# Optimization experiments

Measured on AMD Instinct MI355X. Metric: run time of the kernel, lower is better.

Reference implementation:

```python
import jax, jax.numpy as jnp
import numpy as np

N, Lq, Lk = 4, 4096, 4096
H, P = 16, 128
D = H * P  # 2048


def setup_inputs() -> dict:
    key = jax.random.key(0)
    ks = jax.random.split(key, 7)
    s = 1.0 / np.sqrt(D).astype(np.float32)
    query = jax.random.normal(ks[0], (N, Lq, D), jnp.float32)
    key_t = jax.random.normal(ks[1], (N, Lk, D), jnp.float32)
    Wq = jax.random.normal(ks[2], (D, D), jnp.float32) * s
    Wk = jax.random.normal(ks[3], (D, D), jnp.float32) * s
    Wv = jax.random.normal(ks[4], (D, D), jnp.float32) * s
    query_padding_mask = jax.random.uniform(ks[5], (N, Lq)) < 0.1
    key_padding_mask = jax.random.uniform(ks[6], (N, Lk)) < 0.1
    return {"query": query, "key": key_t, "Wq": Wq, "Wk": Wk, "Wv": Wv,
            "query_padding_mask": query_padding_mask,
            "key_padding_mask": key_padding_mask}


def reference(query, key, Wq, Wk, Wv, query_padding_mask, key_padding_mask):
    n, lq, _ = query.shape
    lk = key.shape[1]
    # torch.nn.Linear(bias=False): y = x @ W^T; split into heads -> (N,H,L,P)
    q = (query @ Wq.T).reshape(n, lq, H, P).transpose(0, 2, 1, 3)
    k = (key @ Wk.T).reshape(n, lk, H, P).transpose(0, 2, 1, 3)
    v = (key @ Wv.T).reshape(n, lk, H, P).transpose(0, 2, 1, 3)
    # _log_exp_kernel(x) = log(1 + exp(x)) = softplus
    pq = jax.nn.softplus(q)
    pk = jax.nn.softplus(k)
    # zero out padded keys so they contribute nothing to numerator/denominator
    pk = jnp.where(key_padding_mask[:, None, :, None], 0.0, pk)
    # linear attention: O(L*d^2) instead of O(L^2*d)
    kv = jnp.einsum("nhkd,nhke->nhde", pk, v)          # (N,H,P,P)
    num = jnp.einsum("nhqd,nhde->nhqe", pq, kv)        # (N,H,Lq,P)
    den = jnp.einsum("nhqd,nhd->nhq", pq, pk.sum(axis=2))[..., None]
    att = num / den
    out = att.transpose(0, 2, 1, 3).reshape(n, lq, H * P)
    # zero out padded query positions
    out = jnp.where(query_padding_mask[..., None], 0.0, out)
    return out
```

## Files before the change

kernel.cpp:

```cpp
#include <hip/hip_runtime.h>
#include <stdint.h>

typedef __attribute__((ext_vector_type(8))) short    bh8;
typedef __attribute__((ext_vector_type(4))) float    fx4;
typedef __attribute__((ext_vector_type(4))) float    f4v;
typedef unsigned short u16;
typedef __attribute__((ext_vector_type(4))) unsigned short u16x4;

#define DEV static __device__ __forceinline__

DEV u16 f2bf(float f) {
  unsigned u = __float_as_uint(f);
  u += 0x7FFFu + ((u >> 16) & 1u);
  return (u16)(u >> 16);
}
DEV float bf2f(u16 s) { return __uint_as_float(((unsigned)s) << 16); }
DEV float softplus_f(float x) { return fmaxf(x, 0.f) + log1pf(expf(-fabsf(x))); }

DEV void gload_lds16(const u16* g, u16* l) {
  __builtin_amdgcn_global_load_lds(
      (const __attribute__((address_space(1))) unsigned int*)g,
      (__attribute__((address_space(3))) unsigned int*)l, 16, 0, 0);
}
DEV void stage2(const u16* s, u16* d) {
  gload_lds16(s, d);
  gload_lds16(s + 131072, d + 4096);
}

__global__ __launch_bounds__(256) void k_cvt(const float* __restrict__ in,
                                             u16* __restrict__ out, int n4) {
  int i = blockIdx.x * 256 + threadIdx.x;
  int stride = gridDim.x * 256;
  for (; i < n4; i += stride) {
    f4v v = ((const f4v*)in)[i];
    u16x4 o;
    o.x = f2bf(v.x); o.y = f2bf(v.y); o.z = f2bf(v.z); o.w = f2bf(v.w);
    ((u16x4*)out)[i] = o;
  }
}


#define MM(a, b, c) __builtin_amdgcn_mfma_f32_16x16x32_bf16(a, b, c, 0, 0, 0)
#define LD(BASE, RR, KS) \
  (*(const bh8*)&lsg[(BASE) + (RR) * 64 + ((((KS) * 32) + ko8) ^ swz)])

#define DECLQ(Q)                                                          \
  fx4 acc##Q##00 = {}, acc##Q##01 = {}, acc##Q##10 = {}, acc##Q##11 = {}, \
      acc##Q##20 = {}, acc##Q##21 = {}, acc##Q##30 = {}, acc##Q##31 = {}

#define DECLFRAGS                                                         \
  bh8 a_00 = {}, a_01 = {}, a_10 = {}, a_11 = {},                         \
      a_20 = {}, a_21 = {}, a_30 = {}, a_31 = {};                         \
  bh8 b0_00 = {}, b0_01 = {}, b0_10 = {}, b0_11 = {};                     \
  bh8 b1_00 = {}, b1_01 = {}, b1_10 = {}, b1_11 = {};

#define LDA4(AB, KS)                                                     \
  a_0##KS = LD(AB, arow0,      KS); a_1##KS = LD(AB, arow0 + 16, KS);    \
  a_2##KS = LD(AB, arow0 + 32, KS); a_3##KS = LD(AB, arow0 + 48, KS);

#define LDB2(BN, BB, KS)                                                 \
  b##BN##_0##KS = LD(BB, brow0,      KS);                                \
  b##BN##_1##KS = LD(BB, brow0 + 16, KS);

#define MFMA8(Q, BN, KS)                                                 \
  acc##Q##00 = MM(a_0##KS, b##BN##_0##KS, acc##Q##00);                   \
  acc##Q##01 = MM(a_0##KS, b##BN##_1##KS, acc##Q##01);                   \
  acc##Q##10 = MM(a_1##KS, b##BN##_0##KS, acc##Q##10);                   \
  acc##Q##11 = MM(a_1##KS, b##BN##_1##KS, acc##Q##11);                   \
  acc##Q##20 = MM(a_2##KS, b##BN##_0##KS, acc##Q##20);                   \
  acc##Q##21 = MM(a_2##KS, b##BN##_1##KS, acc##Q##21);                   \
  acc##Q##30 = MM(a_3##KS, b##BN##_0##KS, acc##Q##30);                   \
  acc##Q##31 = MM(a_3##KS, b##BN##_1##KS, acc##Q##31);

#define KREGION(ABASE, BBASE, DA, DB, SA, SB) {                          \
  stage2(SA,            lsu + (DA));                                     \
  stage2((SA) + 262144, lsu + (DA) + 8192);                              \
  stage2(SB,            lsu + (DB));                                     \
  stage2((SB) + 262144, lsu + (DB) + 8192);                              \
  LDA4(ABASE, 0) LDA4(ABASE, 1)                                          \
  LDB2(0, BBASE, 0) LDB2(0, BBASE, 1)                                    \
  LDB2(1, (BBASE) + 8192, 0) LDB2(1, (BBASE) + 8192, 1)                  \
  __builtin_amdgcn_s_setprio(1);                                         \
  MFMA8(0, 0, 0) MFMA8(0, 0, 1) MFMA8(1, 1, 0) MFMA8(1, 1, 1)            \
  LDA4((ABASE) + 8192, 0) LDA4((ABASE) + 8192, 1)                        \
  MFMA8(2, 0, 0) MFMA8(2, 0, 1) MFMA8(3, 1, 0) MFMA8(3, 1, 1)            \
  __builtin_amdgcn_s_setprio(0);                                         \
  asm volatile("s_waitcnt vmcnt(0)");                                    \
  __builtin_amdgcn_s_barrier();                                          \
}

#define STE(AC, EL, JOFF) {                                                   \
  float v = AC.EL;                                                            \
  if (EPI >= 1) v = softplus_f(v);                                            \
  if (EPI == 2) { if (mask[gi0 + JOFF]) v = 0.f; }                            \
  C[(size_t)(gi0 + JOFF) * 2048 + gj] = f2bf(v);                              \
}
#define ST1(AC, QR, QC, MI, NI) {                                             \
  int gi0 = bm0 + (QR) * 128 + wr * 64 + (MI) * 16 + (lane >> 4) * 4;         \
  int gj  = bn0 + (QC) * 128 + wc * 32 + (NI) * 16 + l15;                     \
  STE(AC, x, 0) STE(AC, y, 1) STE(AC, z, 2) STE(AC, w, 3)                     \
}
#define EPIQ(Q, QR, QC)                                                       \
  ST1(acc##Q##00, QR, QC, 0, 0) ST1(acc##Q##01, QR, QC, 0, 1)                 \
  ST1(acc##Q##10, QR, QC, 1, 0) ST1(acc##Q##11, QR, QC, 1, 1)                 \
  ST1(acc##Q##20, QR, QC, 2, 0) ST1(acc##Q##21, QR, QC, 2, 1)                 \
  ST1(acc##Q##30, QR, QC, 3, 0) ST1(acc##Q##31, QR, QC, 3, 1)

template <int EPI>
__global__ __launch_bounds__(512, 2) void k_gemm256(
    const u16* __restrict__ A, const u16* __restrict__ B, u16* __restrict__ C,
    const int* __restrict__ mask) {
  extern __shared__ u16 lsg[];
  int tid = threadIdx.x, lane = tid & 63, wid = tid >> 6;
  int xcd = blockIdx.x & 7, i = blockIdx.x >> 3;
  int bm0 = (xcd * 8 + (i & 7)) << 8;
  int bn0 = (i >> 3) << 8;
  int wr = wid >> 2, wc = wid & 3;
  int l15 = lane & 15, ko8 = (lane >> 4) * 8;
  int swz = (l15 & 7) << 3;
  int arow0 = wr * 64 + l15, brow0 = wc * 32 + l15;
  int lr = lane >> 3, cg = (lane & 7) ^ lr;
  const u16* srcA = A + (size_t)(bm0 + wid * 8 + lr) * 2048 + cg * 8;
  const u16* srcB = B + (size_t)(bn0 + wid * 8 + lr) * 2048 + cg * 8;
  u16* lsu = lsg + wid * 512;

  DECLQ(0); DECLQ(1); DECLQ(2); DECLQ(3);
  DECLFRAGS

  stage2(srcA,          lsu + 0);
  stage2(srcA + 262144, lsu + 8192);
  stage2(srcB,          lsu + 16384);
  stage2(srcB + 262144, lsu + 24576);
  asm volatile("s_waitcnt vmcnt(0)");
  __builtin_amdgcn_s_barrier();

  for (int it = 0; it < 16; it++) {
    const u16* sA1 = srcA + (2 * it + 1) * 64;
    const u16* sB1 = srcB + (2 * it + 1) * 64;
    int t2 = (2 * it + 2) & 31;
    const u16* sA2 = srcA + t2 * 64;
    const u16* sB2 = srcB + t2 * 64;
    KREGION(0,     16384, 32768, 49152, sA1, sB1)
    KREGION(32768, 49152, 0,     16384, sA2, sB2)
  }

  EPIQ(0, 0, 0)
  EPIQ(1, 0, 1)
  EPIQ(2, 1, 0)
  EPIQ(3, 1, 1)
}

__global__ __launch_bounds__(256, 2) void k_kv2(const u16* __restrict__ pk,
                                                const u16* __restrict__ v,
                                                float* __restrict__ part,
                                                float* __restrict__ spart) {
  int nh = blockIdx.x >> 3, slab = blockIdx.x & 7;
  int n = nh >> 4, h = nh & 15;
  __shared__ u16 lsA[128 * 32];
  __shared__ u16 lsB[128 * 32];
  __shared__ float redS[32][128];
  int tid = threadIdx.x, lane = tid & 63, wid = tid >> 6;
  int wr = wid >> 1, wc = wid & 1;
  int kk = tid >> 3;
  int dg = (tid & 7) * 16;
  size_t rowbase = ((size_t)(n * 4096 + slab * 512) + kk) * 2048 + h * 128 + dg;
  int r = lane & 15, ko = (lane >> 4) * 8;
  fx4 acc[4][4] = {};
  float sA[16];
#pragma unroll
  for (int i = 0; i < 16; i++) sA[i] = 0.f;
  for (int k0 = 0; k0 < 512; k0 += 32) {
    __syncthreads();
    bh8 a0 = *(const bh8*)(pk + rowbase + (size_t)k0 * 2048);
    bh8 a1 = *(const bh8*)(pk + rowbase + (size_t)k0 * 2048 + 8);
    bh8 b0 = *(const bh8*)(v + rowbase + (size_t)k0 * 2048);
    bh8 b1 = *(const bh8*)(v + rowbase + (size_t)k0 * 2048 + 8);
#pragma unroll
    for (int i = 0; i < 8; i++) {
      sA[i] += bf2f((u16)a0[i]);
      sA[8 + i] += bf2f((u16)a1[i]);
    }
#pragma unroll
    for (int i = 0; i < 8; i++) {
      lsA[(dg + i) * 32 + kk] = (u16)a0[i];
      lsA[(dg + 8 + i) * 32 + kk] = (u16)a1[i];
      lsB[(dg + i) * 32 + kk] = (u16)b0[i];
      lsB[(dg + 8 + i) * 32 + kk] = (u16)b1[i];
    }
    __syncthreads();
    bh8 af[4], bfr[4];
#pragma unroll
    for (int mi = 0; mi < 4; mi++)
      af[mi] = *(const bh8*)&lsA[(wr * 64 + mi * 16 + r) * 32 + ko];
#pragma unroll
    for (int ni = 0; ni < 4; ni++)
      bfr[ni] = *(const bh8*)&lsB[(wc * 64 + ni * 16 + r) * 32 + ko];
#pragma unroll
    for (int mi = 0; mi < 4; mi++)
#pragma unroll
      for (int ni = 0; ni < 4; ni++)
        acc[mi][ni] = __builtin_amdgcn_mfma_f32_16x16x32_bf16(af[mi], bfr[ni],
                                                              acc[mi][ni], 0, 0, 0);
  }
#pragma unroll
  for (int mi = 0; mi < 4; mi++)
#pragma unroll
    for (int ni = 0; ni < 4; ni++)
#pragma unroll
      for (int j = 0; j < 4; j++) {
        int d = wr * 64 + mi * 16 + (lane >> 4) * 4 + j;
        int e = wc * 64 + ni * 16 + (lane & 15);
        part[(size_t)blockIdx.x * 16384 + e * 128 + d] = acc[mi][ni][j];
      }
#pragma unroll
  for (int i = 0; i < 16; i++) redS[kk][dg + i] = sA[i];
  __syncthreads();
  if (tid < 128) {
    float s = 0.f;
#pragma unroll
    for (int p = 0; p < 32; p++) s += redS[p][tid];
    spart[blockIdx.x * 128 + tid] = s;
  }
}

__global__ __launch_bounds__(256) void k_red(const float* __restrict__ part,
                                             const float* __restrict__ spart,
                                             u16* __restrict__ kvT,
                                             float* __restrict__ sb) {
  int nh = blockIdx.x, tid = threadIdx.x;
  for (int i = tid; i < 16384; i += 256) {
    float s = 0.f;
#pragma unroll
    for (int sl = 0; sl < 8; sl++) s += part[(size_t)(nh * 8 + sl) * 16384 + i];
    kvT[(size_t)nh * 16384 + i] = f2bf(s);
  }
  if (tid < 128) {
    float s = 0.f;
#pragma unroll
    for (int sl = 0; sl < 8; sl++) s += spart[(nh * 8 + sl) * 128 + tid];
    sb[nh * 128 + tid] = s;
  }
}

__global__ __launch_bounds__(256, 2) void k_att(
    const u16* __restrict__ pq, const u16* __restrict__ kvT,
    const float* __restrict__ s, const int* __restrict__ qmask,
    float* __restrict__ out) {
  int b = blockIdx.x;
  int lt = b & 31, h = (b >> 5) & 15, nb = b >> 9;
  int l0 = lt * 128;
  __shared__ u16 lsQ[128 * 128];
  __shared__ u16 lsKV[128 * 128];
  __shared__ float lsS[128];
  __shared__ float lsDen[128];
  int tid = threadIdx.x, lane = tid & 63, wid = tid >> 6;

  int row = tid >> 1, part = tid & 1;
  const u16* gq = pq + ((size_t)(nb * 4096 + l0 + row)) * 2048 + h * 128 + part * 64;
  const u16* gk = kvT + ((size_t)(nb * 16 + h) * 128 + row) * 128 + part * 64;
  int sw = (row & 7) << 3;
#pragma unroll
  for (int j = 0; j < 8; j++) {
    bh8 vq = *(const bh8*)(gq + j * 8);
    bh8 vk = *(const bh8*)(gk + j * 8);
    int ci = (part * 64 + j * 8) ^ sw;
    *(bh8*)&lsQ[row * 128 + ci] = vq;
    *(bh8*)&lsKV[row * 128 + ci] = vk;
  }
  if (tid < 128) lsS[tid] = s[(nb * 16 + h) * 128 + tid];
  __syncthreads();

  if (tid < 128) {
    int rr = tid, swr = (rr & 7) << 3;
    float dsum = 0.f;
    for (int dd = 0; dd < 128; dd++) {
      int d = (dd + rr) & 127;
      dsum += bf2f(lsQ[rr * 128 + (d ^ swr)]) * lsS[d];
    }
    lsDen[rr] = dsum;
  }
  __syncthreads();

  int wr = wid >> 1, wc = wid & 1;
  int r = lane & 15, ko = (lane >> 4) * 8;
  fx4 acc[4][4] = {};
#pragma unroll
  for (int ks = 0; ks < 4; ks++) {
    bh8 af[4], bfr[4];
#pragma unroll
    for (int mi = 0; mi < 4; mi++) {
      int rw = wr * 64 + mi * 16 + r;
      af[mi] = *(const bh8*)&lsQ[rw * 128 + ((ks * 32 + ko) ^ ((rw & 7) << 3))];
    }
#pragma unroll
    for (int ni = 0; ni < 4; ni++) {
      int rw = wc * 64 + ni * 16 + r;
      bfr[ni] = *(const bh8*)&lsKV[rw * 128 + ((ks * 32 + ko) ^ ((rw & 7) << 3))];
    }
#pragma unroll
    for (int mi = 0; mi < 4; mi++)
#pragma unroll
      for (int ni = 0; ni < 4; ni++)
        acc[mi][ni] = __builtin_amdgcn_mfma_f32_16x16x32_bf16(af[mi], bfr[ni],
                                                              acc[mi][ni], 0, 0, 0);
  }
#pragma unroll
  for (int mi = 0; mi < 4; mi++)
#pragma unroll
    for (int ni = 0; ni < 4; ni++)
#pragma unroll
      for (int j = 0; j < 4; j++) {
        int li = wr * 64 + mi * 16 + (lane >> 4) * 4 + j;
        int e = wc * 64 + ni * 16 + (lane & 15);
        int l = l0 + li;
        float v = qmask[nb * 4096 + l] ? 0.f : acc[mi][ni][j] / lsDen[li];
        out[((size_t)(nb * 4096 + l)) * 2048 + h * 128 + e] = v;
      }
}

extern "C" void kernel_launch(void* const* d_in, const int* in_sizes, int n_in,
                              void* d_out, int out_size, void* d_ws, size_t ws_size,
                              hipStream_t stream) {
  const float* query = (const float*)d_in[0];
  const float* key   = (const float*)d_in[1];
  const float* Wq    = (const float*)d_in[2];
  const float* Wk    = (const float*)d_in[3];
  const float* Wv    = (const float*)d_in[4];
  const int* qmask   = (const int*)d_in[5];
  const int* kmask   = (const int*)d_in[6];
  float* out = (float*)d_out;
  char* ws = (char*)d_ws;

  u16* qb   = (u16*)(ws + 0);
  u16* kb   = (u16*)(ws + 67108864ull);
  u16* Wqb  = (u16*)(ws + 134217728ull);
  u16* Wkb  = (u16*)(ws + 142606336ull);
  u16* Wvb  = (u16*)(ws + 150994944ull);
  u16* pq   = (u16*)(ws + 159383552ull);
  u16* kvT  = (u16*)(ws + 226492416ull);
  float* sb = (float*)(ws + 228589568ull);
  float* kvpart = (float*)(ws + 0);
  float* spart  = (float*)(ws + 33554432ull);
  u16* pk = (u16*)d_out;
  u16* vb = (u16*)d_out + 33554432ull;

  k_cvt<<<2048, 256, 0, stream>>>(query, qb, 33554432 / 4);
  k_cvt<<<2048, 256, 0, stream>>>(key, kb, 33554432 / 4);
  k_cvt<<<512, 256, 0, stream>>>(Wq, Wqb, 4194304 / 4);
  k_cvt<<<512, 256, 0, stream>>>(Wk, Wkb, 4194304 / 4);
  k_cvt<<<512, 256, 0, stream>>>(Wv, Wvb, 4194304 / 4);

  k_gemm256<1><<<512, 512, 131072, stream>>>(qb, Wqb, pq, nullptr);
  k_gemm256<2><<<512, 512, 131072, stream>>>(kb, Wkb, pk, kmask);
  k_gemm256<0><<<512, 512, 131072, stream>>>(kb, Wvb, vb, nullptr);

  k_kv2<<<512, 256, 0, stream>>>(pk, vb, kvpart, spart);
  k_red<<<64, 256, 0, stream>>>(kvpart, spart, kvT, sb);
  k_att<<<2048, 256, 0, stream>>>(pq, kvT, sb, qmask, out);
}
```

Measured before the change: 740.9 us.

## Shrink projection GEMM tiles to 128x128 and merge fp32-to-bf16 conversions

The three projection GEMMs move from 256x256 tiles with 512 threads and 128KB LDS to 128x128 tiles with 256 threads and 64KB LDS, launched as 2048 blocks. Staging and the per-wave B fragment layout change to match. The five separate fp32-to-bf16 conversion launches become one kernel that relies on the workspace buffers being contiguous. Smaller tiles give more blocks and more resident blocks per CU, but each block reuses its loaded data less, so global and L2 traffic per FLOP roughly doubles.

Measured after the change: 819.5 us. 10.6% more time.

```diff
diff --git a/kernel.cpp b/kernel.cpp
--- a/kernel.cpp
+++ b/kernel.cpp
@@ -22,20 +22,31 @@
       (const __attribute__((address_space(1))) unsigned int*)g,
       (__attribute__((address_space(3))) unsigned int*)l, 16, 0, 0);
 }
-DEV void stage2(const u16* s, u16* d) {
+DEV void stage4(const u16* s, u16* d) {
   gload_lds16(s, d);
+  gload_lds16(s + 65536,  d + 2048);
   gload_lds16(s + 131072, d + 4096);
-}
-
-__global__ __launch_bounds__(256) void k_cvt(const float* __restrict__ in,
-                                             u16* __restrict__ out, int n4) {
+  gload_lds16(s + 196608, d + 6144);
+}
+
+__global__ __launch_bounds__(256) void k_cvt_all(
+    const float* __restrict__ q, const float* __restrict__ k,
+    const float* __restrict__ wq, const float* __restrict__ wk,
+    const float* __restrict__ wv, u16* __restrict__ dst) {
+  const int N4 = 19922944;
   int i = blockIdx.x * 256 + threadIdx.x;
   int stride = gridDim.x * 256;
-  for (; i < n4; i += stride) {
-    f4v v = ((const f4v*)in)[i];
+  for (; i < N4; i += stride) {
+    const float* src; int off;
+    if (i < 8388608)        { src = q;  off = i; }
+    else if (i < 16777216)  { src = k;  off = i - 8388608; }
+    else if (i < 17825792)  { src = wq; off = i - 16777216; }
+    else if (i < 18874368)  { src = wk; off = i - 17825792; }
+    else                    { src = wv; off = i - 18874368; }
+    f4v v = ((const f4v*)src)[off];
     u16x4 o;
     o.x = f2bf(v.x); o.y = f2bf(v.y); o.z = f2bf(v.z); o.w = f2bf(v.w);
-    ((u16x4*)out)[i] = o;
+    ((u16x4*)dst)[i] = o;
   }
 }
 
@@ -58,9 +69,9 @@
   a_0##KS = LD(AB, arow0,      KS); a_1##KS = LD(AB, arow0 + 16, KS);    \
   a_2##KS = LD(AB, arow0 + 32, KS); a_3##KS = LD(AB, arow0 + 48, KS);
 
-#define LDB2(BN, BB, KS)                                                 \
-  b##BN##_0##KS = LD(BB, brow0,      KS);                                \
-  b##BN##_1##KS = LD(BB, brow0 + 16, KS);
+#define LDB4(BN, BB, KS)                                                 \
+  b##BN##_0##KS = LD(BB, brow0 + (BN) * 32,      KS);                    \
+  b##BN##_1##KS = LD(BB, brow0 + (BN) * 32 + 16, KS);
 
 #define MFMA8(Q, BN, KS)                                                 \
   acc##Q##00 = MM(a_0##KS, b##BN##_0##KS, acc##Q##00);                   \
@@ -72,21 +83,18 @@
   acc##Q##30 = MM(a_3##KS, b##BN##_0##KS, acc##Q##30);                   \
   acc##Q##31 = MM(a_3##KS, b##BN##_1##KS, acc##Q##31);
 
-#define KREGION(ABASE, BBASE, DA, DB, SA, SB) {                          \
-  stage2(SA,            lsu + (DA));                                     \
-  stage2((SA) + 262144, lsu + (DA) + 8192);                              \
-  stage2(SB,            lsu + (DB));                                     \
-  stage2((SB) + 262144, lsu + (DB) + 8192);                              \
-  LDA4(ABASE, 0) LDA4(ABASE, 1)                                          \
-  LDB2(0, BBASE, 0) LDB2(0, BBASE, 1)                                    \
-  LDB2(1, (BBASE) + 8192, 0) LDB2(1, (BBASE) + 8192, 1)                  \
-  __builtin_amdgcn_s_setprio(1);                                         \
-  MFMA8(0, 0, 0) MFMA8(0, 0, 1) MFMA8(1, 1, 0) MFMA8(1, 1, 1)            \
-  LDA4((ABASE) + 8192, 0) LDA4((ABASE) + 8192, 1)                        \
-  MFMA8(2, 0, 0) MFMA8(2, 0, 1) MFMA8(3, 1, 0) MFMA8(3, 1, 1)            \
-  __builtin_amdgcn_s_setprio(0);                                         \
-  asm volatile("s_waitcnt vmcnt(0)");                                    \
-  __builtin_amdgcn_s_barrier();                                          \
+#define KTILE(AB, BB, SA, SB, DA, DB) {      \
+  stage4(SA, lsu + (DA));                    \
+  stage4(SB, lsu + (DB));                    \
+  LDA4(AB, 0) LDA4(AB, 1)                    \
+  LDB4(0, BB, 0) LDB4(0, BB, 1)              \
+  LDB4(1, BB, 0) LDB4(1, BB, 1)              \
+  __builtin_amdgcn_s_setprio(1);             \
+  MFMA8(0, 0, 0) MFMA8(0, 0, 1)              \
+  MFMA8(1, 1, 0) MFMA8(1, 1, 1)              \
+  __builtin_amdgcn_s_setprio(0);             \
+  asm volatile("s_waitcnt vmcnt(0)");        \
+  __builtin_amdgcn_s_barrier();              \
 }
 
 #define STE(AC, EL, JOFF) {                                                   \
@@ -95,42 +103,40 @@
   if (EPI == 2) { if (mask[gi0 + JOFF]) v = 0.f; }                            \
   C[(size_t)(gi0 + JOFF) * 2048 + gj] = f2bf(v);                              \
 }
-#define ST1(AC, QR, QC, MI, NI) {                                             \
-  int gi0 = bm0 + (QR) * 128 + wr * 64 + (MI) * 16 + (lane >> 4) * 4;         \
-  int gj  = bn0 + (QC) * 128 + wc * 32 + (NI) * 16 + l15;                     \
+#define ST1(AC, MI, NJ) {                                                     \
+  int gi0 = bm0 + wr * 64 + (MI) * 16 + (lane >> 4) * 4;                      \
+  int gj  = bn0 + wc * 64 + (NJ) * 16 + l15;                                  \
   STE(AC, x, 0) STE(AC, y, 1) STE(AC, z, 2) STE(AC, w, 3)                     \
 }
-#define EPIQ(Q, QR, QC)                                                       \
-  ST1(acc##Q##00, QR, QC, 0, 0) ST1(acc##Q##01, QR, QC, 0, 1)                 \
-  ST1(acc##Q##10, QR, QC, 1, 0) ST1(acc##Q##11, QR, QC, 1, 1)                 \
-  ST1(acc##Q##20, QR, QC, 2, 0) ST1(acc##Q##21, QR, QC, 2, 1)                 \
-  ST1(acc##Q##30, QR, QC, 3, 0) ST1(acc##Q##31, QR, QC, 3, 1)
+#define EPIQ(Q, NB)                                                           \
+  ST1(acc##Q##00, 0, NB) ST1(acc##Q##01, 0, (NB) + 1)                         \
+  ST1(acc##Q##10, 1, NB) ST1(acc##Q##11, 1, (NB) + 1)                         \
+  ST1(acc##Q##20, 2, NB) ST1(acc##Q##21, 2, (NB) + 1)                         \
+  ST1(acc##Q##30, 3, NB) ST1(acc##Q##31, 3, (NB) + 1)
 
 template <int EPI>
-__global__ __launch_bounds__(512, 2) void k_gemm256(
+__global__ __launch_bounds__(256, 2) void k_gemm128(
     const u16* __restrict__ A, const u16* __restrict__ B, u16* __restrict__ C,
     const int* __restrict__ mask) {
   extern __shared__ u16 lsg[];
   int tid = threadIdx.x, lane = tid & 63, wid = tid >> 6;
   int xcd = blockIdx.x & 7, i = blockIdx.x >> 3;
-  int bm0 = (xcd * 8 + (i & 7)) << 8;
-  int bn0 = (i >> 3) << 8;
-  int wr = wid >> 2, wc = wid & 3;
+  int bm0 = (xcd * 16 + (i >> 4)) << 7;
+  int bn0 = (i & 15) << 7;
+  int wr = wid >> 1, wc = wid & 1;
   int l15 = lane & 15, ko8 = (lane >> 4) * 8;
   int swz = (l15 & 7) << 3;
-  int arow0 = wr * 64 + l15, brow0 = wc * 32 + l15;
+  int arow0 = wr * 64 + l15, brow0 = wc * 64 + l15;
   int lr = lane >> 3, cg = (lane & 7) ^ lr;
   const u16* srcA = A + (size_t)(bm0 + wid * 8 + lr) * 2048 + cg * 8;
   const u16* srcB = B + (size_t)(bn0 + wid * 8 + lr) * 2048 + cg * 8;
   u16* lsu = lsg + wid * 512;
 
-  DECLQ(0); DECLQ(1); DECLQ(2); DECLQ(3);
+  DECLQ(0); DECLQ(1);
   DECLFRAGS
 
-  stage2(srcA,          lsu + 0);
-  stage2(srcA + 262144, lsu + 8192);
-  stage2(srcB,          lsu + 16384);
-  stage2(srcB + 262144, lsu + 24576);
+  stage4(srcA, lsu + 0);
+  stage4(srcB, lsu + 8192);
   asm volatile("s_waitcnt vmcnt(0)");
   __builtin_amdgcn_s_barrier();
 
@@ -140,14 +146,12 @@
     int t2 = (2 * it + 2) & 31;
     const u16* sA2 = srcA + t2 * 64;
     const u16* sB2 = srcB + t2 * 64;
-    KREGION(0,     16384, 32768, 49152, sA1, sB1)
-    KREGION(32768, 49152, 0,     16384, sA2, sB2)
-  }
-
-  EPIQ(0, 0, 0)
-  EPIQ(1, 0, 1)
-  EPIQ(2, 1, 0)
-  EPIQ(3, 1, 1)
+    KTILE(0,     8192,  sA1, sB1, 16384, 24576)
+    KTILE(16384, 24576, sA2, sB2, 0,     8192)
+  }
+
+  EPIQ(0, 0)
+  EPIQ(1, 2)
 }
 
 __global__ __launch_bounds__(256, 2) void k_kv2(const u16* __restrict__ pk,
@@ -344,15 +348,11 @@
   u16* pk = (u16*)d_out;
   u16* vb = (u16*)d_out + 33554432ull;
 
-  k_cvt<<<2048, 256, 0, stream>>>(query, qb, 33554432 / 4);
-  k_cvt<<<2048, 256, 0, stream>>>(key, kb, 33554432 / 4);
-  k_cvt<<<512, 256, 0, stream>>>(Wq, Wqb, 4194304 / 4);
-  k_cvt<<<512, 256, 0, stream>>>(Wk, Wkb, 4194304 / 4);
-  k_cvt<<<512, 256, 0, stream>>>(Wv, Wvb, 4194304 / 4);
-
-  k_gemm256<1><<<512, 512, 131072, stream>>>(qb, Wqb, pq, nullptr);
-  k_gemm256<2><<<512, 512, 131072, stream>>>(kb, Wkb, pk, kmask);
-  k_gemm256<0><<<512, 512, 131072, stream>>>(kb, Wvb, vb, nullptr);
+  k_cvt_all<<<2048, 256, 0, stream>>>(query, key, Wq, Wk, Wv, qb);
+
+  k_gemm128<1><<<2048, 256, 65536, stream>>>(qb, Wqb, pq, nullptr);
+  k_gemm128<2><<<2048, 256, 65536, stream>>>(kb, Wkb, pk, kmask);
+  k_gemm128<0><<<2048, 256, 65536, stream>>>(kb, Wvb, vb, nullptr);
 
   k_kv2<<<512, 256, 0, stream>>>(pk, vb, kvpart, spart);
   k_red<<<64, 256, 0, stream>>>(kvpart, spart, kvT, sb);
```

## Restructure GEMM main loop into double-buffered register/LDS pipeline and fuse conversions

Applied to the files above, without the earlier changes.

The GEMM main loop is reorganised so that LDS fragment reads for the next k-slice go into a second register set while MFMAs consume the current set, with global-to-LDS staging issued one slice ahead across two LDS buffers. The aim is to hide LDS read latency and global load latency behind matrix-core work instead of waiting inside each region. The five separate fp32-to-bf16 conversion launches are merged into one kernel over a contiguous destination, which removes launch overhead. The cost is a doubled fragment register footprint, which may pressure occupancy at two blocks per CU, plus more delicate waitcnt and barrier ordering.

Result: slower. 807.0 us (+8.9%).

```diff
diff --git a/kernel.cpp b/kernel.cpp
--- a/kernel.cpp
+++ b/kernel.cpp
@@ -27,15 +27,24 @@
   gload_lds16(s + 131072, d + 4096);
 }
 
-__global__ __launch_bounds__(256) void k_cvt(const float* __restrict__ in,
-                                             u16* __restrict__ out, int n4) {
+__global__ __launch_bounds__(256) void k_cvt_all(
+    const float* __restrict__ q, const float* __restrict__ k,
+    const float* __restrict__ wq, const float* __restrict__ wk,
+    const float* __restrict__ wv, u16* __restrict__ dst) {
+  const int N4 = 19922944;
   int i = blockIdx.x * 256 + threadIdx.x;
   int stride = gridDim.x * 256;
-  for (; i < n4; i += stride) {
-    f4v v = ((const f4v*)in)[i];
+  for (; i < N4; i += stride) {
+    const float* src; int off;
+    if (i < 8388608)        { src = q;  off = i; }
+    else if (i < 16777216)  { src = k;  off = i - 8388608; }
+    else if (i < 17825792)  { src = wq; off = i - 16777216; }
+    else if (i < 18874368)  { src = wk; off = i - 17825792; }
+    else                    { src = wv; off = i - 18874368; }
+    f4v v = ((const f4v*)src)[off];
     u16x4 o;
     o.x = f2bf(v.x); o.y = f2bf(v.y); o.z = f2bf(v.z); o.w = f2bf(v.w);
-    ((u16x4*)out)[i] = o;
+    ((u16x4*)dst)[i] = o;
   }
 }
 
@@ -48,45 +57,58 @@
   fx4 acc##Q##00 = {}, acc##Q##01 = {}, acc##Q##10 = {}, acc##Q##11 = {}, \
       acc##Q##20 = {}, acc##Q##21 = {}, acc##Q##30 = {}, acc##Q##31 = {}
 
-#define DECLFRAGS                                                         \
-  bh8 a_00 = {}, a_01 = {}, a_10 = {}, a_11 = {},                         \
-      a_20 = {}, a_21 = {}, a_30 = {}, a_31 = {};                         \
-  bh8 b0_00 = {}, b0_01 = {}, b0_10 = {}, b0_11 = {};                     \
-  bh8 b1_00 = {}, b1_01 = {}, b1_10 = {}, b1_11 = {};
-
-#define LDA4(AB, KS)                                                     \
-  a_0##KS = LD(AB, arow0,      KS); a_1##KS = LD(AB, arow0 + 16, KS);    \
-  a_2##KS = LD(AB, arow0 + 32, KS); a_3##KS = LD(AB, arow0 + 48, KS);
-
-#define LDB2(BN, BB, KS)                                                 \
-  b##BN##_0##KS = LD(BB, brow0,      KS);                                \
-  b##BN##_1##KS = LD(BB, brow0 + 16, KS);
-
-#define MFMA8(Q, BN, KS)                                                 \
-  acc##Q##00 = MM(a_0##KS, b##BN##_0##KS, acc##Q##00);                   \
-  acc##Q##01 = MM(a_0##KS, b##BN##_1##KS, acc##Q##01);                   \
-  acc##Q##10 = MM(a_1##KS, b##BN##_0##KS, acc##Q##10);                   \
-  acc##Q##11 = MM(a_1##KS, b##BN##_1##KS, acc##Q##11);                   \
-  acc##Q##20 = MM(a_2##KS, b##BN##_0##KS, acc##Q##20);                   \
-  acc##Q##21 = MM(a_2##KS, b##BN##_1##KS, acc##Q##21);                   \
-  acc##Q##30 = MM(a_3##KS, b##BN##_0##KS, acc##Q##30);                   \
-  acc##Q##31 = MM(a_3##KS, b##BN##_1##KS, acc##Q##31);
-
-#define KREGION(ABASE, BBASE, DA, DB, SA, SB) {                          \
-  stage2(SA,            lsu + (DA));                                     \
-  stage2((SA) + 262144, lsu + (DA) + 8192);                              \
-  stage2(SB,            lsu + (DB));                                     \
-  stage2((SB) + 262144, lsu + (DB) + 8192);                              \
-  LDA4(ABASE, 0) LDA4(ABASE, 1)                                          \
-  LDB2(0, BBASE, 0) LDB2(0, BBASE, 1)                                    \
-  LDB2(1, (BBASE) + 8192, 0) LDB2(1, (BBASE) + 8192, 1)                  \
-  __builtin_amdgcn_s_setprio(1);                                         \
-  MFMA8(0, 0, 0) MFMA8(0, 0, 1) MFMA8(1, 1, 0) MFMA8(1, 1, 1)            \
-  LDA4((ABASE) + 8192, 0) LDA4((ABASE) + 8192, 1)                        \
-  MFMA8(2, 0, 0) MFMA8(2, 0, 1) MFMA8(3, 1, 0) MFMA8(3, 1, 1)            \
-  __builtin_amdgcn_s_setprio(0);                                         \
-  asm volatile("s_waitcnt vmcnt(0)");                                    \
-  __builtin_amdgcn_s_barrier();                                          \
+#define DECLSET(S)                                                        \
+  bh8 aA##S##0 = {}, aA##S##1 = {}, aA##S##2 = {}, aA##S##3 = {},         \
+      aB##S##0 = {}, aB##S##1 = {}, aB##S##2 = {}, aB##S##3 = {},         \
+      b0##S##0 = {}, b0##S##1 = {}, b1##S##0 = {}, b1##S##1 = {};
+
+#define RD(S, BUF, KS)                                                       \
+  aA##S##0 = LD((BUF),         arow0,      KS);                              \
+  aA##S##1 = LD((BUF),         arow0 + 16, KS);                              \
+  aA##S##2 = LD((BUF),         arow0 + 32, KS);                              \
+  aA##S##3 = LD((BUF),         arow0 + 48, KS);                              \
+  aB##S##0 = LD((BUF) + 8192,  arow0,      KS);                              \
+  aB##S##1 = LD((BUF) + 8192,  arow0 + 16, KS);                              \
+  aB##S##2 = LD((BUF) + 8192,  arow0 + 32, KS);                              \
+  aB##S##3 = LD((BUF) + 8192,  arow0 + 48, KS);                              \
+  b0##S##0 = LD((BUF) + 16384, brow0,      KS);                              \
+  b0##S##1 = LD((BUF) + 16384, brow0 + 16, KS);                              \
+  b1##S##0 = LD((BUF) + 24576, brow0,      KS);                              \
+  b1##S##1 = LD((BUF) + 24576, brow0 + 16, KS);
+
+#define MQ(S, AH, BH, Q)                                                     \
+  acc##Q##00 = MM(a##AH##S##0, b##BH##S##0, acc##Q##00);                     \
+  acc##Q##01 = MM(a##AH##S##0, b##BH##S##1, acc##Q##01);                     \
+  acc##Q##10 = MM(a##AH##S##1, b##BH##S##0, acc##Q##10);                     \
+  acc##Q##11 = MM(a##AH##S##1, b##BH##S##1, acc##Q##11);                     \
+  acc##Q##20 = MM(a##AH##S##2, b##BH##S##0, acc##Q##20);                     \
+  acc##Q##21 = MM(a##AH##S##2, b##BH##S##1, acc##Q##21);                     \
+  acc##Q##30 = MM(a##AH##S##3, b##BH##S##0, acc##Q##30);                     \
+  acc##Q##31 = MM(a##AH##S##3, b##BH##S##1, acc##Q##31);
+#define MFMA32(S) MQ(S, A, 0, 0) MQ(S, A, 1, 1) MQ(S, B, 0, 2) MQ(S, B, 1, 3)
+
+#define STAGE8(SA, SB, DBUF)                                                 \
+  stage2((SA),          lsu + (DBUF));                                       \
+  stage2((SA) + 262144, lsu + (DBUF) + 8192);                                \
+  stage2((SB),          lsu + (DBUF) + 16384);                               \
+  stage2((SB) + 262144, lsu + (DBUF) + 24576);
+
+#define REGION_S0(RS, WS, BUF) {                 \
+  __builtin_amdgcn_s_barrier();                  \
+  RD(WS, BUF, 1)                                 \
+  __builtin_amdgcn_s_setprio(1);                 \
+  MFMA32(RS)                                     \
+  __builtin_amdgcn_s_setprio(0);                 \
+  asm volatile("s_waitcnt lgkmcnt(0)");          \
+  asm volatile("s_waitcnt vmcnt(0)");            \
+}
+#define REGION_S1(RS, WS, BUF, SA, SB) {         \
+  __builtin_amdgcn_s_barrier();                  \
+  STAGE8(SA, SB, BUF)                            \
+  RD(WS, (BUF) ^ 32768, 0)                       \
+  __builtin_amdgcn_s_setprio(1);                 \
+  MFMA32(RS)                                     \
+  __builtin_amdgcn_s_setprio(0);                 \
 }
 
 #define STE(AC, EL, JOFF) {                                                   \
@@ -125,23 +147,23 @@
   u16* lsu = lsg + wid * 512;
 
   DECLQ(0); DECLQ(1); DECLQ(2); DECLQ(3);
-  DECLFRAGS
-
-  stage2(srcA,          lsu + 0);
-  stage2(srcA + 262144, lsu + 8192);
-  stage2(srcB,          lsu + 16384);
-  stage2(srcB + 262144, lsu + 24576);
-  asm volatile("s_waitcnt vmcnt(0)");
+  DECLSET(0) DECLSET(1)
+
+  STAGE8(srcA, srcB, 0)
+  STAGE8(srcA + 64, srcB + 64, 32768)
+  asm volatile("s_waitcnt vmcnt(8)");
   __builtin_amdgcn_s_barrier();
+  RD(0, 0, 0)
 
   for (int it = 0; it < 16; it++) {
-    const u16* sA1 = srcA + (2 * it + 1) * 64;
-    const u16* sB1 = srcB + (2 * it + 1) * 64;
-    int t2 = (2 * it + 2) & 31;
-    const u16* sA2 = srcA + t2 * 64;
-    const u16* sB2 = srcB + t2 * 64;
-    KREGION(0,     16384, 32768, 49152, sA1, sB1)
-    KREGION(32768, 49152, 0,     16384, sA2, sB2)
+    const u16* sA2 = srcA + ((2 * it + 2) & 31) * 64;
+    const u16* sB2 = srcB + ((2 * it + 2) & 31) * 64;
+    const u16* sA3 = srcA + ((2 * it + 3) & 31) * 64;
+    const u16* sB3 = srcB + ((2 * it + 3) & 31) * 64;
+    REGION_S0(0, 1, 0)
+    REGION_S1(1, 0, 0, sA2, sB2)
+    REGION_S0(0, 1, 32768)
+    REGION_S1(1, 0, 32768, sA3, sB3)
   }
 
   EPIQ(0, 0, 0)
@@ -344,11 +366,7 @@
   u16* pk = (u16*)d_out;
   u16* vb = (u16*)d_out + 33554432ull;
 
-  k_cvt<<<2048, 256, 0, stream>>>(query, qb, 33554432 / 4);
-  k_cvt<<<2048, 256, 0, stream>>>(key, kb, 33554432 / 4);
-  k_cvt<<<512, 256, 0, stream>>>(Wq, Wqb, 4194304 / 4);
-  k_cvt<<<512, 256, 0, stream>>>(Wk, Wkb, 4194304 / 4);
-  k_cvt<<<512, 256, 0, stream>>>(Wv, Wvb, 4194304 / 4);
+  k_cvt_all<<<2048, 256, 0, stream>>>(query, key, Wq, Wk, Wv, qb);
 
   k_gemm256<1><<<512, 512, 131072, stream>>>(qb, Wqb, pq, nullptr);
   k_gemm256<2><<<512, 512, 131072, stream>>>(kb, Wkb, pk, kmask);
```
